# Kernel optimization log

Measured on AMD Instinct MI355X. Metric: run time of the kernel, lower is better.

The kernel has to match this reference:

```python
import jax, jax.numpy as jnp
import numpy as np

N_NODES = 100000
N_EDGES = 1600000
IN_F, HID_F, OUT_F = 128, 128, 64


def _sage_conv(x, src, dst, W_self, W_neigh, b, n_nodes):
    # DGL SAGEConv 'mean': out = x @ W_self + mean_{u in N(v)} x_u @ W_neigh + b
    agg = jax.ops.segment_sum(x[src], dst, num_segments=n_nodes)  # [N, d]
    deg = jax.ops.segment_sum(jnp.ones_like(dst, dtype=x.dtype), dst, num_segments=n_nodes)
    neigh = agg / jnp.maximum(deg, 1.0)[:, None]  # zero-in-degree nodes -> 0
    return x @ W_self + neigh @ W_neigh + b


def setup_inputs() -> dict:
    key = jax.random.key(0)
    ks = jax.random.split(key, 8)
    return {
        "features": jax.random.normal(ks[0], (N_NODES, IN_F), dtype=jnp.float32),
        "edge_src": jax.random.randint(ks[1], (N_EDGES,), 0, N_NODES, dtype=jnp.int32),
        "edge_dst": jax.random.randint(ks[2], (N_EDGES,), 0, N_NODES, dtype=jnp.int32),
        "W1_self": jax.random.normal(ks[3], (IN_F, HID_F), dtype=jnp.float32) / np.sqrt(IN_F),
        "W1_neigh": jax.random.normal(ks[4], (IN_F, HID_F), dtype=jnp.float32) / np.sqrt(IN_F),
        "b1": jnp.zeros((HID_F,), dtype=jnp.float32),
        "W2_self": jax.random.normal(ks[5], (HID_F, OUT_F), dtype=jnp.float32) / np.sqrt(HID_F),
        "W2_neigh": jax.random.normal(ks[6], (HID_F, OUT_F), dtype=jnp.float32) / np.sqrt(HID_F),
        "b2": jnp.zeros((OUT_F,), dtype=jnp.float32),
    }


def reference(features, edge_src, edge_dst, W1_self, W1_neigh, b1, W2_self, W2_neigh, b2):
    n = features.shape[0]
    x = _sage_conv(features, edge_src, edge_dst, W1_self, W1_neigh, b1, n)
    x = jax.nn.relu(x)
    # dropout with training=False is a no-op
    return _sage_conv(x, edge_src, edge_dst, W2_self, W2_neigh, b2, n)
```

## Files before the change

kernel.cpp:

```cpp
#include <hip/hip_runtime.h>

#define NODES 100000
#define EDGES 1600000
#define BSH 8
#define NBUCK ((NODES + 255) >> BSH)
#define CHUNK 4096
#define LMAX 8192
#define NCH64 ((NODES + 63) / 64)
#define CONVB 12500
#define MLPGRID 512

using bf16x8 = __attribute__((ext_vector_type(8))) short;
using f32x4  = __attribute__((ext_vector_type(4))) float;
using f32x2  = __attribute__((ext_vector_type(2))) float;

__device__ __forceinline__ unsigned short f2b(float f) {
    unsigned u = __builtin_bit_cast(unsigned, f);
    unsigned r = (u + 0x7FFFu + ((u >> 16) & 1u)) >> 16;
    return (unsigned short)r;
}

__device__ __forceinline__ f32x2 pkadd(f32x2 a, f32x2 b) {
    f32x2 d;
    asm("v_pk_add_f32 %0, %1, %2" : "=v"(d) : "v"(a), "v"(b));
    return d;
}
__device__ __forceinline__ f32x2 pkfma(f32x2 a, f32x2 b, f32x2 c) {
    f32x2 d;
    asm("v_pk_fma_f32 %0, %1, %2, %3" : "=v"(d) : "v"(a), "v"(b), "v"(c));
    return d;
}
__device__ __forceinline__ unsigned cvt2bf(float lo, float hi) {
    unsigned r;
    asm("v_cvt_pk_bf16_f32 %0, %1, %2" : "=v"(r) : "v"(lo), "v"(hi));
    return r;
}

__device__ __forceinline__ bf16x8 gl16(const unsigned short* p) {
    bf16x8 r;
    asm volatile("global_load_dwordx4 %0, %1, off" : "=&v"(r) : "v"(p));
    return r;
}

__device__ __forceinline__ void addpk8(f32x2* a, uint2 v) {
    a[0] = pkadd(a[0], __builtin_amdgcn_cvt_pk_f32_fp8((int)v.x, false));
    a[1] = pkadd(a[1], __builtin_amdgcn_cvt_pk_f32_fp8((int)v.x, true));
    a[2] = pkadd(a[2], __builtin_amdgcn_cvt_pk_f32_fp8((int)v.y, false));
    a[3] = pkadd(a[3], __builtin_amdgcn_cvt_pk_f32_fp8((int)v.y, true));
}


__global__ __launch_bounds__(256) void conv_hist(
    const float* __restrict__ in, unsigned short* __restrict__ outb,
    unsigned char* __restrict__ outq, int n4,
    const float* __restrict__ W1s, const float* __restrict__ W1n,
    const float* __restrict__ W2s, const float* __restrict__ W2n,
    unsigned short* __restrict__ Wt1s, unsigned short* __restrict__ Wt1n,
    unsigned short* __restrict__ Wt2s, unsigned short* __restrict__ Wt2n,
    const int* __restrict__ dst, int* __restrict__ bucket_cnt) {
    int t = threadIdx.x;
    if (blockIdx.x < CONVB) {
        int i = blockIdx.x * 256 + t;
        if (i < n4) {
            float4 v = reinterpret_cast<const float4*>(in)[i];
            uint2 o;
            o.x = (unsigned)f2b(v.x) | ((unsigned)f2b(v.y) << 16);
            o.y = (unsigned)f2b(v.z) | ((unsigned)f2b(v.w) << 16);
            reinterpret_cast<uint2*>(outb)[i] = o;
            int pk = __builtin_amdgcn_cvt_pk_fp8_f32(v.x, v.y, 0, false);
            pk = __builtin_amdgcn_cvt_pk_fp8_f32(v.z, v.w, pk, true);
            reinterpret_cast<unsigned*>(outq)[i] = (unsigned)pk;
        }
        if (i < 16384) {
            int k = i >> 7, n = i & 127;
            Wt1s[n * 128 + k] = f2b(W1s[i]);
            Wt1n[n * 128 + k] = f2b(W1n[i]);
        }
        if (i < 8192) {
            int k = i >> 6, n = i & 63;
            Wt2s[n * 128 + k] = f2b(W2s[i]);
            Wt2n[n * 128 + k] = f2b(W2n[i]);
        }
        return;
    }
    __shared__ int lcnt[512];
    lcnt[t] = 0; lcnt[t + 256] = 0;
    __syncthreads();
    int base = (blockIdx.x - CONVB) * 16384;
    int n = EDGES - base;
    if (n > 16384) n = 16384;
    const int4* d4 = reinterpret_cast<const int4*>(dst + base);
    for (int i = t; i < (n >> 2); i += 256) {
        int4 d = d4[i];
        atomicAdd(&lcnt[d.x >> BSH], 1);
        atomicAdd(&lcnt[d.y >> BSH], 1);
        atomicAdd(&lcnt[d.z >> BSH], 1);
        atomicAdd(&lcnt[d.w >> BSH], 1);
    }
    for (int i = (n & ~3) + t; i < n; i += 256) atomicAdd(&lcnt[dst[base + i] >> BSH], 1);
    __syncthreads();
    if (lcnt[t]) atomicAdd(&bucket_cnt[t], lcnt[t]);
    if (lcnt[t + 256]) atomicAdd(&bucket_cnt[t + 256], lcnt[t + 256]);
}

__global__ void bscan_kernel(const int* __restrict__ bucket_cnt, int* __restrict__ bucket_off,
                             int* __restrict__ gcursor, int* __restrict__ row_ptr) {
    __shared__ int sh[512];
    int t = threadIdx.x;
    int v = (t < NBUCK) ? bucket_cnt[t] : 0;
    sh[t] = v;
    __syncthreads();
    for (int off = 1; off < 512; off <<= 1) {
        int x = (t >= off) ? sh[t - off] : 0;
        __syncthreads();
        sh[t] += x;
        __syncthreads();
    }
    int excl = sh[t] - v;
    if (t < NBUCK) { bucket_off[t] = excl; gcursor[t] = excl; }
    if (t == NBUCK) bucket_off[t] = EDGES;
    if (t == 0) row_ptr[NODES] = EDGES;
}

__global__ __launch_bounds__(256) void binscat_kernel(
    const int* __restrict__ src, const int* __restrict__ dst,
    int* __restrict__ gcursor, unsigned* __restrict__ pairs) {
    __shared__ int cnt[512];
    __shared__ int scn[512];
    __shared__ int gbs[512];
    __shared__ int cur[512];
    __shared__ uint2 stage[CHUNK];
    int t = threadIdx.x;
    int base = blockIdx.x * CHUNK;
    int n = EDGES - base;
    if (n > CHUNK) n = CHUNK;

    cnt[t] = 0; cnt[t + 256] = 0;
    __syncthreads();

    uint2 my[16];
#pragma unroll
    for (int i = 0; i < 16; ++i) {
        int idx = t + i * 256;
        if (idx < n) {
            int d = dst[base + idx];
            int s = src[base + idx];
            my[i] = make_uint2((unsigned)d, (unsigned)s);
            atomicAdd(&cnt[d >> BSH], 1);
        } else {
            my[i] = make_uint2(0xFFFFFFFFu, 0);
        }
    }
    __syncthreads();
    scn[t] = cnt[t]; scn[t + 256] = cnt[t + 256];
    __syncthreads();
    for (int off = 1; off < 512; off <<= 1) {
        int a0 = (t >= off) ? scn[t - off] : 0;
        int a1 = (t + 256 >= off) ? scn[t + 256 - off] : 0;
        __syncthreads();
        scn[t] += a0; scn[t + 256] += a1;
        __syncthreads();
    }
    cur[t] = scn[t] - cnt[t];
    cur[t + 256] = scn[t + 256] - cnt[t + 256];
    __syncthreads();
#pragma unroll
    for (int i = 0; i < 16; ++i) {
        if (my[i].x != 0xFFFFFFFFu) {
            int b = (int)(my[i].x >> BSH);
            int p = atomicAdd(&cur[b], 1);
            stage[p] = my[i];
        }
    }
    for (int b2 = t; b2 < 512; b2 += 256) {
        int c = cnt[b2];
        gbs[b2] = (c > 0 && b2 < NBUCK) ? atomicAdd(&gcursor[b2], c) : 0;
    }
    __syncthreads();
    for (int idx = t; idx < n; idx += 256) {
        uint2 p = stage[idx];
        int b = (int)(p.x >> BSH);
        int excl = scn[b] - cnt[b];
        pairs[gbs[b] + idx - excl] = ((p.x & 255u) << 24) | p.y;
    }
}

__global__ __launch_bounds__(256) void localsort_kernel(
    const unsigned* __restrict__ pairs, const int* __restrict__ bucket_off,
    int* __restrict__ row_ptr, int* __restrict__ src_sorted) {
    __shared__ int cnt[256];
    __shared__ int cur[256];
    __shared__ int stage[LMAX];
    int b = blockIdx.x;
    int t = threadIdx.x;
    int node0 = b << BSH;
    int pbeg = bucket_off[b], pend = bucket_off[b + 1];
    int n = pend - pbeg;
    cnt[t] = 0;
    __syncthreads();
    for (int e = pbeg + t; e < pend; e += 256)
        atomicAdd(&cnt[(int)(pairs[e] >> 24)], 1);
    __syncthreads();
    int v = cnt[t];
    cur[t] = v;
    __syncthreads();
    for (int off = 1; off < 256; off <<= 1) {
        int x = (t >= off) ? cur[t - off] : 0;
        __syncthreads();
        cur[t] += x;
        __syncthreads();
    }
    int excl = cur[t] - v;
    int node = node0 + t;
    if (node < NODES) row_ptr[node] = pbeg + excl;
    cur[t] = excl;
    __syncthreads();
    if (n <= LMAX) {
        for (int e = pbeg + t; e < pend; e += 256) {
            unsigned p = pairs[e];
            int pos = atomicAdd(&cur[(int)(p >> 24)], 1);
            stage[pos] = (int)(p & 0xFFFFFFu);
        }
        __syncthreads();
        for (int i = t; i < n; i += 256) src_sorted[pbeg + i] = stage[i];
    } else {
        for (int e = pbeg + t; e < pend; e += 256) {
            unsigned p = pairs[e];
            int pos = atomicAdd(&cur[(int)(p >> 24)], 1);
            src_sorted[pbeg + pos] = (int)(p & 0xFFFFFFu);
        }
    }
}


__global__ __launch_bounds__(256) void agg128_fp8(
    const unsigned char* __restrict__ xq, const int* __restrict__ row_ptr,
    const int* __restrict__ srcs, unsigned short* __restrict__ out) {
    int wave = (blockIdx.x * 256 + threadIdx.x) >> 6;
    int lane = threadIdx.x & 63;
    int sl = lane & 15;
    int n = wave * 4 + (lane >> 4);
    if (n >= NODES) return;
    int beg = row_ptr[n], end = row_ptr[n + 1];
    int gb = lane & 48;

    f32x2 A0[4], A1[4];
#pragma unroll
    for (int i = 0; i < 4; ++i) { A0[i] = {0.f, 0.f}; A1[i] = {0.f, 0.f}; }

    const unsigned char* xs = xq + sl * 8;
    for (int base = beg; base < end; base += 16) {
        int idx = base + sl;
        int sv = (idx < end) ? srcs[idx] : NODES;
        uint2 vv[8], ww[8];
#pragma unroll
        for (int j = 0; j < 8; ++j) {
            int s = __shfl(sv, gb + j, 64);
            vv[j] = *reinterpret_cast<const uint2*>(xs + (size_t)s * 128);
        }
#pragma unroll
        for (int j = 0; j < 8; ++j) {
            int s = __shfl(sv, gb + 8 + j, 64);
            ww[j] = *reinterpret_cast<const uint2*>(xs + (size_t)s * 128);
        }
#pragma unroll
        for (int j = 0; j < 8; ++j) addpk8((j & 1) ? A1 : A0, vv[j]);
#pragma unroll
        for (int j = 0; j < 8; ++j) addpk8((j & 1) ? A0 : A1, ww[j]);
    }

    float inv = 1.0f / fmaxf((float)(end - beg), 1.0f);
    f32x2 iv = {inv, inv};
    f32x2 z = {0.f, 0.f};
    f32x2 r0 = pkfma(pkadd(A0[0], A1[0]), iv, z);
    f32x2 r1 = pkfma(pkadd(A0[1], A1[1]), iv, z);
    f32x2 r2 = pkfma(pkadd(A0[2], A1[2]), iv, z);
    f32x2 r3 = pkfma(pkadd(A0[3], A1[3]), iv, z);
    uint4 o;
    o.x = cvt2bf(r0[0], r0[1]);
    o.y = cvt2bf(r1[0], r1[1]);
    o.z = cvt2bf(r2[0], r2[1]);
    o.w = cvt2bf(r3[0], r3[1]);
    *reinterpret_cast<uint4*>(out + (size_t)n * 128 + sl * 8) = o;
}

__global__ __launch_bounds__(256) void agg64_add8(
    const unsigned char* __restrict__ xq, const int* __restrict__ row_ptr,
    const int* __restrict__ srcs, float* __restrict__ out) {
    int wave = (blockIdx.x * 256 + threadIdx.x) >> 6;
    int lane = threadIdx.x & 63;
    int sl = lane & 7;
    int n = wave * 8 + (lane >> 3);
    if (n >= NODES) return;
    int beg = row_ptr[n], end = row_ptr[n + 1];
    int gb = lane & 56;

    f32x2 A0[4], A1[4];
#pragma unroll
    for (int i = 0; i < 4; ++i) { A0[i] = {0.f, 0.f}; A1[i] = {0.f, 0.f}; }

    const unsigned char* xs = xq + sl * 8;
    for (int base = beg; base < end; base += 16) {
        int i0 = base + sl, i1 = base + 8 + sl;
        int sv0 = (i0 < end) ? srcs[i0] : NODES;
        int sv1 = (i1 < end) ? srcs[i1] : NODES;
        uint2 vv[16];
#pragma unroll
        for (int j = 0; j < 8; ++j) {
            int s = __shfl(sv0, gb + j, 64);
            vv[j] = *reinterpret_cast<const uint2*>(xs + (size_t)s * 64);
        }
#pragma unroll
        for (int j = 0; j < 8; ++j) {
            int s = __shfl(sv1, gb + j, 64);
            vv[8 + j] = *reinterpret_cast<const uint2*>(xs + (size_t)s * 64);
        }
#pragma unroll
        for (int j = 0; j < 16; ++j) addpk8((j & 1) ? A1 : A0, vv[j]);
    }

    float inv = 1.0f / fmaxf((float)(end - beg), 1.0f);
    f32x2 iv = {inv, inv};
    float* op = out + (size_t)n * 64 + sl * 8;
    f32x2 r0 = *reinterpret_cast<f32x2*>(op);
    f32x2 r1 = *reinterpret_cast<f32x2*>(op + 2);
    f32x2 r2 = *reinterpret_cast<f32x2*>(op + 4);
    f32x2 r3 = *reinterpret_cast<f32x2*>(op + 6);
    r0 = pkfma(pkadd(A0[0], A1[0]), iv, r0);
    r1 = pkfma(pkadd(A0[1], A1[1]), iv, r1);
    r2 = pkfma(pkadd(A0[2], A1[2]), iv, r2);
    r3 = pkfma(pkadd(A0[3], A1[3]), iv, r3);
    *reinterpret_cast<f32x2*>(op) = r0;
    *reinterpret_cast<f32x2*>(op + 2) = r1;
    *reinterpret_cast<f32x2*>(op + 4) = r2;
    *reinterpret_cast<f32x2*>(op + 6) = r3;
}


__global__ __launch_bounds__(256, 2) void fused_mlp(
    const unsigned short* __restrict__ featb, const unsigned short* __restrict__ agg,
    const unsigned short* __restrict__ Wt1s, const unsigned short* __restrict__ Wt1n,
    const float* __restrict__ b1, const unsigned short* __restrict__ Wt2s,
    const unsigned short* __restrict__ Wt2n, const float* __restrict__ b2,
    unsigned char* __restrict__ x1h8, float* __restrict__ outp) {
    __shared__ __align__(16) unsigned short w1t[32768];
    __shared__ __align__(16) unsigned short x1t[64 * 128];
    int wid = threadIdx.x >> 6, lane = threadIdx.x & 63;
    int l15 = lane & 15, quad = lane >> 4;

    {
        const uint4* gs = reinterpret_cast<const uint4*>(Wt1s);
        const uint4* gn = reinterpret_cast<const uint4*>(Wt1n);
        uint4* ls = reinterpret_cast<uint4*>(w1t);
        uint4* ln = ls + 2048;
#pragma unroll
        for (int i = 0; i < 8; ++i) {
            int g = threadIdx.x + i * 256;
            int sw = (g & ~15) | ((g & 15) ^ ((g >> 4) & 7));
            ls[sw] = gs[g];
            ln[sw] = gn[g];
        }
    }

    int col2 = wid * 16 + l15;
    bf16x8 B2s[4], B2n[4];
#pragma unroll
    for (int k = 0; k < 4; ++k) {
        B2s[k] = gl16(Wt2s + (size_t)col2 * 128 + k * 32 + quad * 8);
        B2n[k] = gl16(Wt2n + (size_t)col2 * 128 + k * 32 + quad * 8);
    }
    float bv2 = b2[col2];
    float bv1[8];
#pragma unroll
    for (int nt = 0; nt < 8; ++nt) bv1[nt] = b1[nt * 16 + l15];

    auto loadA = [&](int cc, bf16x8 (&Afd)[4], bf16x8 (&Aad)[4]) {
        int r = cc * 64 + wid * 16 + l15;
        if (r >= NODES) r = NODES - 1;
        const unsigned short* fp = featb + (size_t)r * 128 + quad * 8;
        const unsigned short* ap = agg + (size_t)r * 128 + quad * 8;
#pragma unroll
        for (int k = 0; k < 4; ++k) {
            Afd[k] = *reinterpret_cast<const bf16x8*>(fp + k * 32);
            Aad[k] = *reinterpret_cast<const bf16x8*>(ap + k * 32);
        }
    };

    bf16x8 Af[4], Aa[4];
    int c = blockIdx.x;
    if (c < NCH64) loadA(c, Af, Aa);

    asm volatile("s_waitcnt vmcnt(0)" ::: "memory");
    __builtin_amdgcn_sched_barrier(0);
    __syncthreads();

    int swz = l15 & 7;

    for (; c < NCH64; c += MLPGRID) {
        int rbase = c * 64;
        int cn = c + MLPGRID;

        f32x4 acc[8];
#pragma unroll
        for (int nt = 0; nt < 8; ++nt) acc[nt] = {0.f, 0.f, 0.f, 0.f};
#pragma unroll
        for (int k = 0; k < 4; ++k) {
            int so = ((k * 4 + quad) ^ swz) << 3;
#pragma unroll
            for (int nt = 0; nt < 8; ++nt) {
                const unsigned short* wb = w1t + (size_t)(nt * 16 + l15) * 128;
                bf16x8 b1s = *reinterpret_cast<const bf16x8*>(wb + so);
                bf16x8 b1n = *reinterpret_cast<const bf16x8*>(wb + 16384 + so);
                acc[nt] = __builtin_amdgcn_mfma_f32_16x16x32_bf16(Af[k], b1s, acc[nt], 0, 0, 0);
                acc[nt] = __builtin_amdgcn_mfma_f32_16x16x32_bf16(Aa[k], b1n, acc[nt], 0, 0, 0);
            }
        }

        bf16x8 Pf[4], Pa[4];
        if (cn < NCH64) loadA(cn, Pf, Pa);

#pragma unroll
        for (int nt = 0; nt < 8; ++nt)
#pragma unroll
            for (int rr = 0; rr < 4; ++rr) {
                float v = fmaxf(acc[nt][rr] + bv1[nt], 0.f);
                int row = wid * 16 + quad * 4 + rr;
                int col = nt * 16 + l15;
                int slot = (col >> 3) ^ (row & 7);
                x1t[row * 128 + slot * 8 + (col & 7)] = f2b(v);
            }
        __syncthreads();

        f32x4 a2s[4], a2n[4];
#pragma unroll
        for (int mt = 0; mt < 4; ++mt) { a2s[mt] = {0.f, 0.f, 0.f, 0.f}; a2n[mt] = {0.f, 0.f, 0.f, 0.f}; }
#pragma unroll
        for (int k = 0; k < 4; ++k)
#pragma unroll
            for (int mt = 0; mt < 4; ++mt) {
                int row = mt * 16 + l15;
                int slot = (k * 4 + quad) ^ (row & 7);
                bf16x8 a = *reinterpret_cast<const bf16x8*>(x1t + row * 128 + slot * 8);
                a2s[mt] = __builtin_amdgcn_mfma_f32_16x16x32_bf16(a, B2s[k], a2s[mt], 0, 0, 0);
                a2n[mt] = __builtin_amdgcn_mfma_f32_16x16x32_bf16(a, B2n[k], a2n[mt], 0, 0, 0);
            }
        __syncthreads();

#pragma unroll
        for (int mt = 0; mt < 4; ++mt)
#pragma unroll
            for (int rr = 0; rr < 4; ++rr) {
                int row = rbase + mt * 16 + quad * 4 + rr;
                if (row < NODES) {
                    float vn = a2n[mt][rr];
                    int pk = __builtin_amdgcn_cvt_pk_fp8_f32(vn, vn, 0, false);
                    x1h8[(size_t)row * 64 + col2] = (unsigned char)(pk & 0xFF);
                    outp[(size_t)row * 64 + col2] = a2s[mt][rr] + bv2;
                }
            }

        if (cn < NCH64) {
#pragma unroll
            for (int k = 0; k < 4; ++k) {
                Af[k] = Pf[k];
                Aa[k] = Pa[k];
            }
        }
    }
}


extern "C" void kernel_launch(void* const* d_in, const int* in_sizes, int n_in,
                              void* d_out, int out_size, void* d_ws, size_t ws_size,
                              hipStream_t stream) {
    const float* features = (const float*)d_in[0];
    const int* esrc = (const int*)d_in[1];
    const int* edst = (const int*)d_in[2];
    const float* W1s = (const float*)d_in[3];
    const float* W1n = (const float*)d_in[4];
    const float* b1  = (const float*)d_in[5];
    const float* W2s = (const float*)d_in[6];
    const float* W2n = (const float*)d_in[7];
    const float* b2  = (const float*)d_in[8];
    float* out = (float*)d_out;

    char* ws = (char*)d_ws;
    size_t off = 0;
    auto alloc = [&](size_t bytes) {
        void* p = ws + off;
        off += (bytes + 255) & ~(size_t)255;
        return p;
    };
    int* bucket_cnt = (int*)alloc(512 * 4);
    int* bucket_off = (int*)alloc(512 * 4);
    int* gcursor    = (int*)alloc(512 * 4);
    int* row_ptr    = (int*)alloc((size_t)(NODES + 1) * 4);
    int* src_sorted = (int*)alloc((size_t)EDGES * 4);
    unsigned* pairs = (unsigned*)alloc((size_t)EDGES * 4);
    unsigned short* featb = (unsigned short*)alloc((size_t)NODES * 128 * 2);
    unsigned char*  feat8 = (unsigned char*)alloc((size_t)(NODES + 1) * 128);
    unsigned short* agg1  = (unsigned short*)alloc((size_t)NODES * 128 * 2);
    unsigned char*  x1h8  = (unsigned char*)alloc((size_t)(NODES + 1) * 64);
    unsigned short* Wt1s  = (unsigned short*)alloc(16384 * 2);
    unsigned short* Wt1n  = (unsigned short*)alloc(16384 * 2);
    unsigned short* Wt2s  = (unsigned short*)alloc(8192 * 2);
    unsigned short* Wt2n  = (unsigned short*)alloc(8192 * 2);

    hipMemsetAsync(bucket_cnt, 0, 512 * 4, stream);
    hipMemsetAsync(feat8 + (size_t)NODES * 128, 0, 128, stream);
    hipMemsetAsync(x1h8 + (size_t)NODES * 64, 0, 64, stream);

    conv_hist<<<CONVB + (EDGES + 16383) / 16384, 256, 0, stream>>>(
        features, featb, feat8, NODES * 128 / 4, W1s, W1n, W2s, W2n,
        Wt1s, Wt1n, Wt2s, Wt2n, edst, bucket_cnt);

    bscan_kernel<<<1, 512, 0, stream>>>(bucket_cnt, bucket_off, gcursor, row_ptr);
    binscat_kernel<<<(EDGES + CHUNK - 1) / CHUNK, 256, 0, stream>>>(esrc, edst, gcursor, pairs);
    localsort_kernel<<<NBUCK, 256, 0, stream>>>(pairs, bucket_off, row_ptr, src_sorted);

    agg128_fp8<<<(NODES / 4 * 64 + 255) / 256, 256, 0, stream>>>(feat8, row_ptr, src_sorted, agg1);

    fused_mlp<<<MLPGRID, 256, 0, stream>>>(featb, agg1, Wt1s, Wt1n, b1, Wt2s, Wt2n, b2, x1h8, out);

    agg64_add8<<<(NODES / 8 * 64 + 255) / 256, 256, 0, stream>>>(x1h8, row_ptr, src_sorted, out);
}
```

Before: 237.4 us.

## Split fp8 layer-1 aggregation into 8 feature slices with edge-parallel lanes

Restructures the 128-wide fp8 neighbor aggregation so each block handles one 16-byte feature slice for 32 nodes. Each node gets 8 lanes that each walk a strided subset of edges, followed by an xor-shuffle reduction. Slicing features across blocks is meant to shrink the gathered working set per block for better cache locality and to give wider 16-byte loads. The cost is reading each edge list 8 times, extra shuffle reductions, and only 2 of 8 lanes writing output.

```diff
diff --git a/kernel.cpp b/kernel.cpp
--- a/kernel.cpp
+++ b/kernel.cpp
@@ -7,6 +7,7 @@
 #define CHUNK 4096
 #define LMAX 8192
 #define NCH64 ((NODES + 63) / 64)
+#define NCH32 ((NODES + 31) / 32)
 #define CONVB 12500
 #define MLPGRID 512
 
@@ -236,52 +237,77 @@
 __global__ __launch_bounds__(256) void agg128_fp8(
     const unsigned char* __restrict__ xq, const int* __restrict__ row_ptr,
     const int* __restrict__ srcs, unsigned short* __restrict__ out) {
-    int wave = (blockIdx.x * 256 + threadIdx.x) >> 6;
+    int bid = blockIdx.x;
+    int s = bid & 7;
+    int chunk = bid >> 3;
     int lane = threadIdx.x & 63;
-    int sl = lane & 15;
-    int n = wave * 4 + (lane >> 4);
+    int sl = lane & 7;
+    int n = chunk * 32 + ((int)(threadIdx.x >> 6)) * 8 + (lane >> 3);
     if (n >= NODES) return;
     int beg = row_ptr[n], end = row_ptr[n + 1];
-    int gb = lane & 48;
-
-    f32x2 A0[4], A1[4];
-#pragma unroll
-    for (int i = 0; i < 4; ++i) { A0[i] = {0.f, 0.f}; A1[i] = {0.f, 0.f}; }
-
-    const unsigned char* xs = xq + sl * 8;
-    for (int base = beg; base < end; base += 16) {
-        int idx = base + sl;
-        int sv = (idx < end) ? srcs[idx] : NODES;
-        uint2 vv[8], ww[8];
-#pragma unroll
-        for (int j = 0; j < 8; ++j) {
-            int s = __shfl(sv, gb + j, 64);
-            vv[j] = *reinterpret_cast<const uint2*>(xs + (size_t)s * 128);
-        }
-#pragma unroll
-        for (int j = 0; j < 8; ++j) {
-            int s = __shfl(sv, gb + 8 + j, 64);
-            ww[j] = *reinterpret_cast<const uint2*>(xs + (size_t)s * 128);
-        }
-#pragma unroll
-        for (int j = 0; j < 8; ++j) addpk8((j & 1) ? A1 : A0, vv[j]);
-#pragma unroll
-        for (int j = 0; j < 8; ++j) addpk8((j & 1) ? A0 : A1, ww[j]);
+
+    f32x2 A0[4], A1[4], B0[4], B1[4];
+#pragma unroll
+    for (int i = 0; i < 4; ++i) {
+        A0[i] = {0.f, 0.f}; A1[i] = {0.f, 0.f};
+        B0[i] = {0.f, 0.f}; B1[i] = {0.f, 0.f};
+    }
+
+    const unsigned char* xs = xq + s * 16;
+    int e = beg + sl;
+    for (; e + 8 < end; e += 16) {
+        int s0 = srcs[e];
+        int s1 = srcs[e + 8];
+        uint4 v0 = *reinterpret_cast<const uint4*>(xs + (size_t)s0 * 128);
+        uint4 v1 = *reinterpret_cast<const uint4*>(xs + (size_t)s1 * 128);
+        addpk8(A0, make_uint2(v0.x, v0.y));
+        addpk8(A1, make_uint2(v0.z, v0.w));
+        addpk8(B0, make_uint2(v1.x, v1.y));
+        addpk8(B1, make_uint2(v1.z, v1.w));
+    }
+    if (e < end) {
+        int s0 = srcs[e];
+        uint4 v0 = *reinterpret_cast<const uint4*>(xs + (size_t)s0 * 128);
+        addpk8(A0, make_uint2(v0.x, v0.y));
+        addpk8(A1, make_uint2(v0.z, v0.w));
+    }
+
+#pragma unroll
+    for (int i = 0; i < 4; ++i) {
+        A0[i] = pkadd(A0[i], B0[i]);
+        A1[i] = pkadd(A1[i], B1[i]);
+    }
+#pragma unroll
+    for (int i = 0; i < 4; ++i) {
+        f32x2 t;
+#pragma unroll
+        for (int h = 1; h <= 4; h <<= 1) {
+            t[0] = __shfl_xor(A0[i][0], h, 64);
+            t[1] = __shfl_xor(A0[i][1], h, 64);
+            A0[i] = pkadd(A0[i], t);
+            t[0] = __shfl_xor(A1[i][0], h, 64);
+            t[1] = __shfl_xor(A1[i][1], h, 64);
+            A1[i] = pkadd(A1[i], t);
+        }
     }
 
     float inv = 1.0f / fmaxf((float)(end - beg), 1.0f);
-    f32x2 iv = {inv, inv};
-    f32x2 z = {0.f, 0.f};
-    f32x2 r0 = pkfma(pkadd(A0[0], A1[0]), iv, z);
-    f32x2 r1 = pkfma(pkadd(A0[1], A1[1]), iv, z);
-    f32x2 r2 = pkfma(pkadd(A0[2], A1[2]), iv, z);
-    f32x2 r3 = pkfma(pkadd(A0[3], A1[3]), iv, z);
-    uint4 o;
-    o.x = cvt2bf(r0[0], r0[1]);
-    o.y = cvt2bf(r1[0], r1[1]);
-    o.z = cvt2bf(r2[0], r2[1]);
-    o.w = cvt2bf(r3[0], r3[1]);
-    *reinterpret_cast<uint4*>(out + (size_t)n * 128 + sl * 8) = o;
+    unsigned short* op = out + (size_t)n * 128 + s * 16;
+    if (sl == 0) {
+        uint4 o0;
+        o0.x = cvt2bf(A0[0][0] * inv, A0[0][1] * inv);
+        o0.y = cvt2bf(A0[1][0] * inv, A0[1][1] * inv);
+        o0.z = cvt2bf(A0[2][0] * inv, A0[2][1] * inv);
+        o0.w = cvt2bf(A0[3][0] * inv, A0[3][1] * inv);
+        *reinterpret_cast<uint4*>(op) = o0;
+    } else if (sl == 1) {
+        uint4 o1;
+        o1.x = cvt2bf(A1[0][0] * inv, A1[0][1] * inv);
+        o1.y = cvt2bf(A1[1][0] * inv, A1[1][1] * inv);
+        o1.z = cvt2bf(A1[2][0] * inv, A1[2][1] * inv);
+        o1.w = cvt2bf(A1[3][0] * inv, A1[3][1] * inv);
+        *reinterpret_cast<uint4*>(op + 8) = o1;
+    }
 }
 
 __global__ __launch_bounds__(256) void agg64_add8(
@@ -518,7 +544,7 @@
     binscat_kernel<<<(EDGES + CHUNK - 1) / CHUNK, 256, 0, stream>>>(esrc, edst, gcursor, pairs);
     localsort_kernel<<<NBUCK, 256, 0, stream>>>(pairs, bucket_off, row_ptr, src_sorted);
 
-    agg128_fp8<<<(NODES / 4 * 64 + 255) / 256, 256, 0, stream>>>(feat8, row_ptr, src_sorted, agg1);
+    agg128_fp8<<<8 * NCH32, 256, 0, stream>>>(feat8, row_ptr, src_sorted, agg1);
 
     fused_mlp<<<MLPGRID, 256, 0, stream>>>(featb, agg1, Wt1s, Wt1n, b1, Wt2s, Wt2n, b2, x1h8, out);
 
```

Result: slower. 381.7 us (+60.8%).
